# Performance work log

Hardware: AMD Instinct MI355X
Metric: run time of the kernel (lower is better)

## Reference

```python
import jax, jax.numpy as jnp
import numpy as np

D = 1024
H = 16
FF = 4096
B = 2
L = 2048
EPS = 1e-5


def setup_inputs() -> dict:
    key = jax.random.key(0)
    ks = jax.random.split(key, 12)
    s = 0.02
    return {
        "x": jax.random.normal(ks[0], (B, L, D), dtype=jnp.float32),
        "ln1_g": jnp.ones((D,), jnp.float32),
        "ln1_b": jnp.zeros((D,), jnp.float32),
        "qkv_w": jax.random.normal(ks[1], (D, 3 * D), dtype=jnp.float32) * s,
        "proj_w": jax.random.normal(ks[2], (D, D), dtype=jnp.float32) * s,
        "proj_b": jnp.zeros((D,), jnp.float32),
        "ln2_g": jnp.ones((D,), jnp.float32),
        "ln2_b": jnp.zeros((D,), jnp.float32),
        "w1": jax.random.normal(ks[3], (D, FF), dtype=jnp.float32) * s,
        "b1": jnp.zeros((FF,), jnp.float32),
        "w2": jax.random.normal(ks[4], (FF, D), dtype=jnp.float32) * s,
        "b2": jnp.zeros((D,), jnp.float32),
    }


def _layernorm(x, g, b):
    mu = jnp.mean(x, axis=-1, keepdims=True)
    var = jnp.var(x, axis=-1, keepdims=True)
    return (x - mu) * jax.lax.rsqrt(var + EPS) * g + b


def _attn(x, qkv_w, proj_w, proj_b):
    Bv, Lv, Dv = x.shape
    dk = Dv // H
    qkv = x @ qkv_w  # [B,L,3D]
    q, k, v = jnp.split(qkv, 3, axis=-1)

    def split(t):
        return t.reshape(Bv, Lv, H, dk).transpose(0, 2, 1, 3)  # [B,H,L,dk]

    q, k, v = map(split, (q, k, v))
    scores = jnp.einsum("bhqd,bhkd->bhqk", q, k) / np.sqrt(dk)
    attn = jax.nn.softmax(scores, axis=-1)
    out = jnp.einsum("bhqk,bhkd->bhqd", attn, v)
    out = out.transpose(0, 2, 1, 3).reshape(Bv, Lv, Dv)
    return out @ proj_w + proj_b


def reference(x, ln1_g, ln1_b, qkv_w, proj_w, proj_b, ln2_g, ln2_b, w1, b1, w2, b2):
    x = x + _attn(_layernorm(x, ln1_g, ln1_b), qkv_w, proj_w, proj_b)
    h = _layernorm(x, ln2_g, ln2_b)
    h = jax.nn.gelu(h @ w1 + b1, approximate=False) @ w2 + b2
    return x + h
```

## Files before the change

### kernel.cpp

```cpp
#include <hip/hip_runtime.h>
#include <cstdint>
#include <cstddef>

typedef __attribute__((ext_vector_type(8))) short bf16x8;
typedef __attribute__((ext_vector_type(4))) short bf16x4;
typedef __attribute__((ext_vector_type(4))) float f32x4;

__device__ __forceinline__ uint16_t f2bf(float f) {
    uint32_t u = __float_as_uint(f);
    u += 0x7FFFu + ((u >> 16) & 1u);
    return (uint16_t)(u >> 16);
}
__device__ __forceinline__ uint32_t bfr(float f) {
    return (__float_as_uint(f) + 0x8000u) >> 16;
}

__device__ __forceinline__ f32x4 mfma16(bf16x8 a, bf16x8 b, f32x4 c) {
    return __builtin_amdgcn_mfma_f32_16x16x32_bf16(a, b, c, 0, 0, 0);
}

__device__ __forceinline__ void async_copy16(const void* g, void* l) {
    __builtin_amdgcn_global_load_lds(
        (__attribute__((address_space(1))) void*)g,
        (__attribute__((address_space(3))) void*)l, 16, 0, 0);
}

template <int N> __device__ __forceinline__ void waitvm() {
    if constexpr (N == 0) asm volatile("s_waitcnt vmcnt(0)" ::: "memory");
    else if constexpr (N == 3) asm volatile("s_waitcnt vmcnt(3)" ::: "memory");
    else if constexpr (N == 4) asm volatile("s_waitcnt vmcnt(4)" ::: "memory");
    else if constexpr (N == 6) asm volatile("s_waitcnt vmcnt(6)" ::: "memory");
    else if constexpr (N == 8) asm volatile("s_waitcnt vmcnt(8)" ::: "memory");
    else if constexpr (N == 9) asm volatile("s_waitcnt vmcnt(9)" ::: "memory");
    else if constexpr (N == 12) asm volatile("s_waitcnt vmcnt(12)" ::: "memory");
}
__device__ __forceinline__ void fence_sched() {
    asm volatile("" ::: "memory");
    __builtin_amdgcn_sched_barrier(0);
}

typedef __attribute__((address_space(3))) const uint16_t lds_cu16;
__device__ __forceinline__ bf16x4 tr_read(lds_cu16* p) {
    bf16x4 d;
    asm volatile("ds_read_b64_tr_b16 %0, %1" : "=v"(d) : "v"(p));
    return d;
}
__device__ __forceinline__ bf16x8 cat8(bf16x4 lo, bf16x4 hi) {
    return __builtin_shufflevector(lo, hi, 0, 1, 2, 3, 4, 5, 6, 7);
}

__global__ __launch_bounds__(256) void transpose_cast(const float* __restrict__ W,
                                                      uint16_t* __restrict__ Wt,
                                                      int K, int N) {
    __shared__ uint16_t tile[32][33];
    const int n0 = blockIdx.x * 32, k0 = blockIdx.y * 32;
    const int tx = threadIdx.x, ty = threadIdx.y;
#pragma unroll
    for (int j = 0; j < 4; ++j) {
        int k = k0 + ty + j * 8;
        tile[ty + j * 8][tx] = f2bf(W[(size_t)k * N + n0 + tx]);
    }
    __syncthreads();
#pragma unroll
    for (int j = 0; j < 4; ++j) {
        int n = n0 + ty + j * 8;
        Wt[(size_t)n * K + k0 + tx] = tile[tx][ty + j * 8];
    }
}

__global__ __launch_bounds__(256) void ln_kernel(const float* __restrict__ x,
                                                 const float* __restrict__ g,
                                                 const float* __restrict__ b,
                                                 uint16_t* __restrict__ out) {
    const int row = blockIdx.x;
    const int t = threadIdx.x;
    const float* xr = x + (size_t)row * 1024;
    float4 v = *(const float4*)(xr + t * 4);
    float s = v.x + v.y + v.z + v.w;
    float s2 = v.x * v.x + v.y * v.y + v.z * v.z + v.w * v.w;
#pragma unroll
    for (int off = 1; off < 64; off <<= 1) {
        s += __shfl_xor(s, off);
        s2 += __shfl_xor(s2, off);
    }
    __shared__ float sh[8];
    const int wv = t >> 6;
    if ((t & 63) == 0) { sh[wv] = s; sh[4 + wv] = s2; }
    __syncthreads();
    s = sh[0] + sh[1] + sh[2] + sh[3];
    s2 = sh[4] + sh[5] + sh[6] + sh[7];
    const float mu = s * (1.f / 1024.f);
    const float var = s2 * (1.f / 1024.f) - mu * mu;
    const float rs = rsqrtf(var + 1e-5f);
    float4 gg = *(const float4*)(g + t * 4);
    float4 bb = *(const float4*)(b + t * 4);
    ushort4 ov;
    ov.x = f2bf((v.x - mu) * rs * gg.x + bb.x);
    ov.y = f2bf((v.y - mu) * rs * gg.y + bb.y);
    ov.z = f2bf((v.z - mu) * rs * gg.z + bb.z);
    ov.w = f2bf((v.w - mu) * rs * gg.w + bb.w);
    *(ushort4*)(out + (size_t)row * 1024 + t * 4) = ov;
}

template <int EPI, int BM, int BN>
__global__ __launch_bounds__(256, 2) void rgemm(const uint16_t* __restrict__ A,
                                                const uint16_t* __restrict__ Bt,
                                                const float* __restrict__ bias,
                                                const float* __restrict__ resid,
                                                void* __restrict__ outp,
                                                int M, int N, int K) {
    constexpr int MI = BM / 32, NI = BN / 32;
    constexpr int AW = BM / 64;
    constexpr int LPS = AW + 2;
    __shared__ uint16_t As[4][BM * 32];
    __shared__ uint16_t Bs[4][BN * 32];
    const int t = threadIdx.x, lane = t & 63, w = t >> 6;
    const int l16 = lane & 15, lhi = lane >> 4;
    const int wr = w >> 1, wc = w & 1;
    const int m0 = blockIdx.x * BM, n0 = blockIdx.y * BN;

    f32x4 acc[MI][NI];
    const f32x4 z = {0.f, 0.f, 0.f, 0.f};
#pragma unroll
    for (int mi = 0; mi < MI; ++mi)
#pragma unroll
        for (int ni = 0; ni < NI; ++ni) acc[mi][ni] = z;

    const int lrow = lane >> 2;
    const int lg = lane & 3;
    const uint16_t* Abase = A + (size_t)m0 * K;
    const uint16_t* Bbase = Bt + (size_t)n0 * K;

    auto stage = [&](int ti, int s) {
        const int kt = ti * 32;
#pragma unroll
        for (int j = 0; j < AW; ++j) {
            int rb = w * (BM / 4) + j * 16;
            int r = rb + lrow;
            int g = lg ^ ((r >> 1) & 3);
            async_copy16(Abase + (size_t)r * K + kt + g * 8, &As[s][rb * 32]);
        }
#pragma unroll
        for (int j = 0; j < 2; ++j) {
            int rb = w * (BN / 4) + j * 16;
            int r = rb + lrow;
            int g = lg ^ ((r >> 1) & 3);
            async_copy16(Bbase + (size_t)r * K + kt + g * 8, &Bs[s][rb * 32]);
        }
    };

    auto compute = [&](int s) {
        bf16x8 af[MI], bfr[NI];
#pragma unroll
        for (int mi = 0; mi < MI; ++mi) {
            int r = wr * (BM / 2) + mi * 16 + l16;
            af[mi] = *(const bf16x8*)&As[s][r * 32 + ((lhi ^ ((r >> 1) & 3)) << 3)];
        }
#pragma unroll
        for (int ni = 0; ni < NI; ++ni) {
            int r = wc * (BN / 2) + ni * 16 + l16;
            bfr[ni] = *(const bf16x8*)&Bs[s][r * 32 + ((lhi ^ ((r >> 1) & 3)) << 3)];
        }
        __builtin_amdgcn_s_setprio(1);
#pragma unroll
        for (int mi = 0; mi < MI; ++mi)
#pragma unroll
            for (int ni = 0; ni < NI; ++ni)
                acc[mi][ni] = mfma16(af[mi], bfr[ni], acc[mi][ni]);
        __builtin_amdgcn_s_setprio(0);
    };

    const int nt = K / 32;
    stage(0, 0); stage(1, 1); stage(2, 2); stage(3, 3);

    for (int ti = 0; ti < nt; ++ti) {
        const int rem = nt - 1 - ti;
        if (rem >= 3) waitvm<3 * LPS>();
        else if (rem == 2) waitvm<2 * LPS>();
        else if (rem == 1) waitvm<LPS>();
        else waitvm<0>();
        __builtin_amdgcn_s_barrier();
        fence_sched();
        compute(ti & 3);
        __builtin_amdgcn_s_barrier();
        fence_sched();
        if (ti + 4 < nt) stage(ti + 4, ti & 3);
    }

#pragma unroll
    for (int mi = 0; mi < MI; ++mi) {
#pragma unroll
        for (int ni = 0; ni < NI; ++ni) {
#pragma unroll
            for (int e = 0; e < 4; ++e) {
                int gm = m0 + wr * (BM / 2) + mi * 16 + 4 * lhi + e;
                int gn = n0 + wc * (BN / 2) + ni * 16 + l16;
                float v = acc[mi][ni][e];
                if constexpr (EPI == 0) {
                    ((uint16_t*)outp)[(size_t)gm * N + gn] = f2bf(v);
                } else if constexpr (EPI == 1) {
                    v += bias[gn] + resid[(size_t)gm * N + gn];
                    ((float*)outp)[(size_t)gm * N + gn] = v;
                } else {
                    v += bias[gn];
                    float gl = 0.5f * v * (1.f + erff(v * 0.70710678118f));
                    ((uint16_t*)outp)[(size_t)gm * N + gn] = f2bf(gl);
                }
            }
        }
    }
}

__global__ __launch_bounds__(256) void attn_kernel(const uint16_t* __restrict__ qkv,
                                                   uint16_t* __restrict__ aout) {
    __shared__ uint16_t Kt[2][64 * 64];
    __shared__ uint16_t Vs[2][64 * 64];
    __shared__ uint16_t Pq[4][16 * 64];
    const int qt = blockIdx.x, h = blockIdx.y, b = blockIdx.z;
    const int t = threadIdx.x, lane = t & 63, w = t >> 6;
    const int l16 = lane & 15, lhi = lane >> 4;
    const int q0 = qt * 64;
    const uint16_t* base = qkv + (size_t)(b * 2048) * 3072 + h * 64;

    bf16x8 aq[2];
    {
        const uint16_t* qp = base + (size_t)(q0 + w * 16 + l16) * 3072;
        aq[0] = *(const bf16x8*)(qp + 8 * lhi);
        aq[1] = *(const bf16x8*)(qp + 32 + 8 * lhi);
    }

    const int krow = lane >> 3;
    const int kgs = ((lane & 7) ^ krow) << 3;
    const int vkk = ((lane >> 5) << 2) | ((lane >> 1) & 3);
    const int vd  = (((lane >> 3) & 3) << 4) | ((lane & 1) << 3);

    auto stage = [&](int tile, int bufi) {
        const uint16_t* kb = base + (size_t)(tile * 64) * 3072 + 1024;
        const uint16_t* vb = base + (size_t)(tile * 64) * 3072 + 2048;
#pragma unroll
        for (int p = 0; p < 2; ++p) {
            int r0 = w * 16 + p * 8;
            async_copy16(kb + (size_t)(r0 + krow) * 3072 + kgs, &Kt[bufi][r0 * 64]);
        }
#pragma unroll
        for (int p = 0; p < 2; ++p) {
            int i = w * 2 + p;
            async_copy16(vb + (size_t)(i * 8 + vkk) * 3072 + vd, &Vs[bufi][i * 512]);
        }
    };

    const f32x4 z = {0.f, 0.f, 0.f, 0.f};
    f32x4 oaccT[4];
#pragma unroll
    for (int n = 0; n < 4; ++n) oaccT[n] = z;
    float lrun = 0.f;
    const float cs = 0.18033688f;

    stage(0, 0);
    __syncthreads();

    for (int tile = 0; tile < 32; ++tile) {
        const int cur = tile & 1;
        if (tile + 1 < 32) stage(tile + 1, cur ^ 1);

        f32x4 sacc[4];
#pragma unroll
        for (int nk = 0; nk < 4; ++nk) sacc[nk] = z;
#pragma unroll
        for (int nk = 0; nk < 4; ++nk) {
#pragma unroll
            for (int kh = 0; kh < 2; ++kh) {
                const int gk = kh * 4 + lhi;
                const int rr = nk * 16 + l16;
                bf16x8 bk = *(const bf16x8*)&Kt[cur][rr * 64 + ((gk ^ (l16 & 7)) << 3)];
                sacc[nk] = mfma16(bk, aq[kh], sacc[nk]);
            }
        }

        float p[4][4];
        float ps = 0.f;
#pragma unroll
        for (int nk = 0; nk < 4; ++nk)
#pragma unroll
            for (int e = 0; e < 4; ++e) {
                float pe = exp2f(sacc[nk][e] * cs);
                p[nk][e] = pe;
                ps += pe;
            }
        ps += __shfl_xor(ps, 16);
        ps += __shfl_xor(ps, 32);
        lrun += ps;

#pragma unroll
        for (int nk = 0; nk < 4; ++nk) {
            uint2 pk;
            pk.x = bfr(p[nk][0]) | (bfr(p[nk][1]) << 16);
            pk.y = bfr(p[nk][2]) | (bfr(p[nk][3]) << 16);
            const int g = nk * 2 + (lhi >> 1);
            *(uint2*)&Pq[w][l16 * 64 + ((g ^ (l16 & 7)) << 3) + ((lhi & 1) << 2)] = pk;
        }
        asm volatile("s_waitcnt lgkmcnt(0)" ::: "memory");
        __builtin_amdgcn_sched_barrier(0);

        bf16x8 pa[2];
#pragma unroll
        for (int kh = 0; kh < 2; ++kh) {
            const int gk = kh * 4 + lhi;
            pa[kh] = *(const bf16x8*)&Pq[w][l16 * 64 + ((gk ^ (l16 & 7)) << 3)];
        }
        lds_cu16* vtb = (lds_cu16*)&Vs[cur][0];
        bf16x8 bv[4][2];
#pragma unroll
        for (int n = 0; n < 4; ++n) {
#pragma unroll
            for (int kh = 0; kh < 2; ++kh) {
                const int gk = kh * 4 + lhi;
                bf16x4 lo = tr_read(vtb + ((gk * 2) << 8) + (n << 6) + l16);
                bf16x4 hi = tr_read(vtb + ((gk * 2 + 1) << 8) + (n << 6) + l16);
                bv[n][kh] = cat8(lo, hi);
            }
        }
        asm volatile("s_waitcnt lgkmcnt(0)" ::: "memory");
        __builtin_amdgcn_sched_barrier(0);

#pragma unroll
        for (int n = 0; n < 4; ++n)
#pragma unroll
            for (int kh = 0; kh < 2; ++kh)
                oaccT[n] = mfma16(bv[n][kh], pa[kh], oaccT[n]);

        __syncthreads();
    }

    const float rl = 1.0f / lrun;
    const size_t orow = (size_t)(b * 2048 + q0 + w * 16 + l16) * 1024 + h * 64;
#pragma unroll
    for (int n = 0; n < 4; ++n) {
        ushort4 ov;
        ov.x = f2bf(oaccT[n][0] * rl);
        ov.y = f2bf(oaccT[n][1] * rl);
        ov.z = f2bf(oaccT[n][2] * rl);
        ov.w = f2bf(oaccT[n][3] * rl);
        *(ushort4*)&aout[orow + n * 16 + 4 * lhi] = ov;
    }
}

extern "C" void kernel_launch(void* const* d_in, const int* in_sizes, int n_in,
                              void* d_out, int out_size, void* d_ws, size_t ws_size,
                              hipStream_t stream) {
    const float* x      = (const float*)d_in[0];
    const float* ln1_g  = (const float*)d_in[1];
    const float* ln1_b  = (const float*)d_in[2];
    const float* qkv_w  = (const float*)d_in[3];
    const float* proj_w = (const float*)d_in[4];
    const float* proj_b = (const float*)d_in[5];
    const float* ln2_g  = (const float*)d_in[6];
    const float* ln2_b  = (const float*)d_in[7];
    const float* w1     = (const float*)d_in[8];
    const float* b1     = (const float*)d_in[9];
    const float* w2     = (const float*)d_in[10];
    const float* b2     = (const float*)d_in[11];
    float* out = (float*)d_out;

    char* ws = (char*)d_ws;
    size_t off = 0;
    auto alloc = [&](size_t bytes) {
        void* p = ws + off;
        off += (bytes + 255) & ~(size_t)255;
        return p;
    };
    uint16_t* wqkv_t  = (uint16_t*)alloc((size_t)3072 * 1024 * 2);
    uint16_t* wproj_t = (uint16_t*)alloc((size_t)1024 * 1024 * 2);
    uint16_t* w1_t    = (uint16_t*)alloc((size_t)4096 * 1024 * 2);
    uint16_t* w2_t    = (uint16_t*)alloc((size_t)1024 * 4096 * 2);
    float*    x2      = (float*)   alloc((size_t)4096 * 1024 * 4);
    uint16_t* lnb     = (uint16_t*)alloc((size_t)4096 * 1024 * 2);
    uint16_t* qkvb    = (uint16_t*)alloc((size_t)4096 * 3072 * 2);
    uint16_t* attnb   = (uint16_t*)alloc((size_t)4096 * 1024 * 2);
    uint16_t* h1      = qkvb;

    dim3 tb(32, 8, 1);
    transpose_cast<<<dim3(3072 / 32, 1024 / 32), tb, 0, stream>>>(qkv_w, wqkv_t, 1024, 3072);
    transpose_cast<<<dim3(1024 / 32, 1024 / 32), tb, 0, stream>>>(proj_w, wproj_t, 1024, 1024);
    transpose_cast<<<dim3(4096 / 32, 1024 / 32), tb, 0, stream>>>(w1, w1_t, 1024, 4096);
    transpose_cast<<<dim3(1024 / 32, 4096 / 32), tb, 0, stream>>>(w2, w2_t, 4096, 1024);

    ln_kernel<<<4096, 256, 0, stream>>>(x, ln1_g, ln1_b, lnb);
    rgemm<0, 128, 128><<<dim3(32, 24), 256, 0, stream>>>(lnb, wqkv_t, nullptr, nullptr, qkvb, 4096, 3072, 1024);
    attn_kernel<<<dim3(32, 16, 2), 256, 0, stream>>>(qkvb, attnb);
    rgemm<1, 64, 128><<<dim3(64, 8), 256, 0, stream>>>(attnb, wproj_t, proj_b, x, x2, 4096, 1024, 1024);
    ln_kernel<<<4096, 256, 0, stream>>>(x2, ln2_g, ln2_b, lnb);
    rgemm<2, 128, 128><<<dim3(32, 32), 256, 0, stream>>>(lnb, w1_t, b1, nullptr, h1, 4096, 4096, 1024);
    rgemm<1, 64, 128><<<dim3(64, 8), 256, 0, stream>>>(h1, w2_t, b2, x2, out, 4096, 1024, 4096);
}
```

Baseline: 296.7 us.

## Add 256x256-tile 512-thread GEMM for QKV and FC1 projections

Adds a new GEMM kernel with 256x256 output tiles, 8 waves per block, a 64-deep K step with double-buffered async global-to-LDS copies and XOR-swizzled LDS, and s_setprio around the MFMA bursts. The QKV and FC1 GEMMs now use it, and the old rgemm is trimmed to its residual-add epilogue. The aim is more data reuse per block and fewer LDS/global loads per MFMA. The cost is about 128KB of LDS per block, so only one block fits per CU. The QKV grid also shrinks to 192 blocks, which may leave CUs idle and expose load latency with only two stages.

New measurement: 292.1 us. No clear change (-1.6%).

```diff
diff --git a/kernel.cpp b/kernel.cpp
--- a/kernel.cpp
+++ b/kernel.cpp
@@ -102,6 +102,95 @@
     *(ushort4*)(out + (size_t)row * 1024 + t * 4) = ov;
 }
 
+template <int EPI>
+__global__ __launch_bounds__(512, 2) void gemm256(const uint16_t* __restrict__ A,
+                                                  const uint16_t* __restrict__ Bt,
+                                                  const float* __restrict__ bias,
+                                                  void* __restrict__ outp,
+                                                  int M, int N, int K) {
+    __shared__ uint16_t As[2][256 * 64];
+    __shared__ uint16_t Bs[2][256 * 64];
+    const int t = threadIdx.x, lane = t & 63, w = t >> 6;
+    const int l16 = lane & 15, lhi = lane >> 4;
+    const int wm = w >> 2, wn = w & 3;
+    const int m0 = blockIdx.x * 256, n0 = blockIdx.y * 256;
+
+    f32x4 acc[8][4];
+    const f32x4 z = {0.f, 0.f, 0.f, 0.f};
+#pragma unroll
+    for (int mi = 0; mi < 8; ++mi)
+#pragma unroll
+        for (int ni = 0; ni < 4; ++ni) acc[mi][ni] = z;
+
+    const int srow = lane >> 3;
+    const int sgs = ((lane & 7) ^ srow) << 3;
+    const uint16_t* Ab = A + (size_t)m0 * K;
+    const uint16_t* Bb = Bt + (size_t)n0 * K;
+
+    auto stage = [&](int ti, int b) {
+        const int kt = ti * 64;
+#pragma unroll
+        for (int j = 0; j < 4; ++j) {
+            int r0 = w * 32 + j * 8;
+            async_copy16(Ab + (size_t)(r0 + srow) * K + kt + sgs, &As[b][r0 * 64]);
+        }
+#pragma unroll
+        for (int j = 0; j < 4; ++j) {
+            int r0 = w * 32 + j * 8;
+            async_copy16(Bb + (size_t)(r0 + srow) * K + kt + sgs, &Bs[b][r0 * 64]);
+        }
+    };
+
+    const int nt = K / 64;
+    stage(0, 0);
+    __syncthreads();
+
+    for (int ti = 0; ti < nt; ++ti) {
+        const int p = ti & 1;
+        if (ti + 1 < nt) stage(ti + 1, p ^ 1);
+#pragma unroll
+        for (int kh = 0; kh < 2; ++kh) {
+            const int gk = kh * 4 + lhi;
+            const int gsw = (gk ^ (l16 & 7)) << 3;
+            bf16x8 af[8], bf[4];
+#pragma unroll
+            for (int mi = 0; mi < 8; ++mi)
+                af[mi] = *(const bf16x8*)&As[p][(wm * 128 + mi * 16 + l16) * 64 + gsw];
+#pragma unroll
+            for (int ni = 0; ni < 4; ++ni)
+                bf[ni] = *(const bf16x8*)&Bs[p][(wn * 64 + ni * 16 + l16) * 64 + gsw];
+            __builtin_amdgcn_s_setprio(1);
+#pragma unroll
+            for (int mi = 0; mi < 8; ++mi)
+#pragma unroll
+                for (int ni = 0; ni < 4; ++ni)
+                    acc[mi][ni] = mfma16(af[mi], bf[ni], acc[mi][ni]);
+            __builtin_amdgcn_s_setprio(0);
+        }
+        __syncthreads();
+    }
+
+#pragma unroll
+    for (int mi = 0; mi < 8; ++mi) {
+#pragma unroll
+        for (int ni = 0; ni < 4; ++ni) {
+#pragma unroll
+            for (int e = 0; e < 4; ++e) {
+                int gm = m0 + wm * 128 + mi * 16 + 4 * lhi + e;
+                int gn = n0 + wn * 64 + ni * 16 + l16;
+                float v = acc[mi][ni][e];
+                if constexpr (EPI == 0) {
+                    ((uint16_t*)outp)[(size_t)gm * N + gn] = f2bf(v);
+                } else {
+                    v += bias[gn];
+                    float gl = 0.5f * v * (1.f + erff(v * 0.70710678118f));
+                    ((uint16_t*)outp)[(size_t)gm * N + gn] = f2bf(gl);
+                }
+            }
+        }
+    }
+}
+
 template <int EPI, int BM, int BN>
 __global__ __launch_bounds__(256, 2) void rgemm(const uint16_t* __restrict__ A,
                                                 const uint16_t* __restrict__ Bt,
@@ -196,16 +285,8 @@
                 int gm = m0 + wr * (BM / 2) + mi * 16 + 4 * lhi + e;
                 int gn = n0 + wc * (BN / 2) + ni * 16 + l16;
                 float v = acc[mi][ni][e];
-                if constexpr (EPI == 0) {
-                    ((uint16_t*)outp)[(size_t)gm * N + gn] = f2bf(v);
-                } else if constexpr (EPI == 1) {
-                    v += bias[gn] + resid[(size_t)gm * N + gn];
-                    ((float*)outp)[(size_t)gm * N + gn] = v;
-                } else {
-                    v += bias[gn];
-                    float gl = 0.5f * v * (1.f + erff(v * 0.70710678118f));
-                    ((uint16_t*)outp)[(size_t)gm * N + gn] = f2bf(gl);
-                }
+                v += bias[gn] + resid[(size_t)gm * N + gn];
+                ((float*)outp)[(size_t)gm * N + gn] = v;
             }
         }
     }
@@ -386,10 +467,10 @@
     transpose_cast<<<dim3(1024 / 32, 4096 / 32), tb, 0, stream>>>(w2, w2_t, 4096, 1024);
 
     ln_kernel<<<4096, 256, 0, stream>>>(x, ln1_g, ln1_b, lnb);
-    rgemm<0, 128, 128><<<dim3(32, 24), 256, 0, stream>>>(lnb, wqkv_t, nullptr, nullptr, qkvb, 4096, 3072, 1024);
+    gemm256<0><<<dim3(16, 12), 512, 0, stream>>>(lnb, wqkv_t, nullptr, qkvb, 4096, 3072, 1024);
     attn_kernel<<<dim3(32, 16, 2), 256, 0, stream>>>(qkvb, attnb);
     rgemm<1, 64, 128><<<dim3(64, 8), 256, 0, stream>>>(attnb, wproj_t, proj_b, x, x2, 4096, 1024, 1024);
     ln_kernel<<<4096, 256, 0, stream>>>(x2, ln2_g, ln2_b, lnb);
-    rgemm<2, 128, 128><<<dim3(32, 32), 256, 0, stream>>>(lnb, w1_t, b1, nullptr, h1, 4096, 4096, 1024);
+    gemm256<2><<<dim3(16, 16), 512, 0, stream>>>(lnb, w1_t, b1, h1, 4096, 4096, 1024);
     rgemm<1, 64, 128><<<dim3(64, 8), 256, 0, stream>>>(h1, w2_t, b2, x2, out, 4096, 1024, 4096);
 }
```
